# Kernel tuning notes

Measured on AMD Instinct MI355X. Metric: run time of the kernel, lower is better.

The kernel has to match this reference:

```python
import jax, jax.numpy as jnp
import numpy as np

MODEL_SIZE = 512
HEADS = 8
T = 2048
B = 2


def setup_inputs() -> dict:
    key = jax.random.key(0)
    ks = jax.random.split(key, 10)
    E = MODEL_SIZE
    w = 0.02  # weight init scale for numerical stability
    return {
        "input": jax.random.normal(ks[0], (T, B, E), jnp.float32),
        "pos": jax.random.normal(ks[1], (T, 1, E), jnp.float32),
        "in_proj_weight": jax.random.normal(ks[2], (3 * E, E), jnp.float32) * w,
        "out_proj_weight": jax.random.normal(ks[3], (E, E), jnp.float32) * w,
        "pos_proj_weight": jax.random.normal(ks[4], (E, E), jnp.float32) * w,
        "in_proj_bias": jax.random.normal(ks[5], (3 * E,), jnp.float32) * w,
        "out_proj_bias": jax.random.normal(ks[6], (E,), jnp.float32) * w,
        "pos_proj_bias": jax.random.normal(ks[7], (E,), jnp.float32) * w,
        "r_w_bias": jax.random.normal(ks[8], (HEADS, E // HEADS), jnp.float32) * w,
        "r_r_bias": jax.random.normal(ks[9], (HEADS, E // HEADS), jnp.float32) * w,
    }


def _rel_shift(x):
    # x: [B, H, T, R] -> Transformer-XL relative shift
    b, h, t, r = x.shape
    x = jnp.pad(x, ((0, 0), (0, 0), (0, 0), (1, 0)))  # [B,H,T,R+1]
    x = x.reshape(b, h, r + 1, t)[:, :, 1:, :]        # drop first row
    return x.reshape(b, h, t, r)


def reference(input, pos, in_proj_weight, out_proj_weight, pos_proj_weight,
              in_proj_bias, out_proj_bias, pos_proj_bias, r_w_bias, r_r_bias):
    t, b, e = input.shape
    h = r_w_bias.shape[0]
    d = e // h
    scale = 1.0 / np.sqrt(d).astype(np.float32)

    # fused QKV projection (time-first layout [T,B,E])
    qkv = input @ in_proj_weight.T + in_proj_bias          # [T,B,3E]
    q, k, v = jnp.split(qkv, 3, axis=-1)
    q = q.reshape(t, b, h, d)
    k = k.reshape(t, b, h, d)
    v = v.reshape(t, b, h, d)

    # relative position projection (pos batch dim is 1)
    r = (pos[:, 0] @ pos_proj_weight.T + pos_proj_bias).reshape(-1, h, d)  # [R,H,D]

    # content (AC) and position (BD) scores
    ac = jnp.einsum('tbhd,sbhd->bhts', q + r_w_bias, k)    # [B,H,T,T]
    bd = jnp.einsum('tbhd,rhd->bhtr', q + r_r_bias, r)     # [B,H,T,R]
    bd = _rel_shift(bd)[..., :t]

    attn = jax.nn.softmax((ac + bd) * scale, axis=-1)      # [B,H,T,T]
    ctx = jnp.einsum('bhts,sbhd->tbhd', attn, v).reshape(t, b, e)
    return ctx @ out_proj_weight.T + out_proj_bias
```

## Files before the change

### kernel.cpp

```cpp
#include <hip/hip_runtime.h>

#define T_SEQ 2048
#define BATCH 2
#define HEADS 8
#define DHEAD 64
#define EMB   512

typedef __attribute__((ext_vector_type(8))) short short8;
typedef __attribute__((ext_vector_type(4))) float floatx4;
typedef __attribute__((ext_vector_type(8))) unsigned short ushort8;
typedef __attribute__((ext_vector_type(4))) unsigned short ushort4v;

__device__ __forceinline__ unsigned short f2b(float f) {
    union { float f; unsigned u; } v; v.f = f;
    unsigned r = v.u + 0x7fffu + ((v.u >> 16) & 1u);
    return (unsigned short)(r >> 16);
}
__device__ __forceinline__ unsigned short f2bt(float f) {
    union { float f; unsigned u; } v; v.f = f;
    return (unsigned short)(v.u >> 16);
}
__device__ __forceinline__ float b2f(unsigned short s) {
    union { unsigned u; float f; } v; v.u = ((unsigned)s) << 16; return v.f;
}
__device__ __forceinline__ short8 ld_frag(const unsigned short* p) {
    ushort4v lo = *(const ushort4v*)p;
    ushort4v hi = *(const ushort4v*)(p + 4);
    short8 r;
    r[0] = lo[0]; r[1] = lo[1]; r[2] = lo[2]; r[3] = lo[3];
    r[4] = hi[0]; r[5] = hi[1]; r[6] = hi[2]; r[7] = hi[3];
    return r;
}
__device__ __forceinline__ void st8(unsigned short* p, ushort8 v) {
    ushort4v lo = { v[0], v[1], v[2], v[3] };
    ushort4v hi = { v[4], v[5], v[6], v[7] };
    *(ushort4v*)p = lo;
    *(ushort4v*)(p + 4) = hi;
}
#define MFMA16(a, b, c) __builtin_amdgcn_mfma_f32_16x16x32_bf16(a, b, c, 0, 0, 0)

__global__ __launch_bounds__(256)
void cvt_all(const float* __restrict__ s0, const float* __restrict__ s1,
             const float* __restrict__ s2, const float* __restrict__ s3,
             const float* __restrict__ s4,
             unsigned short* __restrict__ d0, unsigned short* __restrict__ d1,
             unsigned short* __restrict__ d2, unsigned short* __restrict__ d3,
             unsigned short* __restrict__ d4)
{
    const int i = blockIdx.x * 256 + threadIdx.x;
    const float* s; unsigned short* d; int off;
    if      (i <  524288) { s = s0; d = d0; off = i; }
    else if (i <  786432) { s = s1; d = d1; off = i -  524288; }
    else if (i <  983040) { s = s2; d = d2; off = i -  786432; }
    else if (i < 1048576) { s = s3; d = d3; off = i -  983040; }
    else if (i < 1114112) { s = s4; d = d4; off = i - 1048576; }
    else return;
    const float4 v = ((const float4*)s)[off];
    ushort4v o = { f2b(v.x), f2b(v.y), f2b(v.z), f2b(v.w) };
    ((ushort4v*)d)[off] = o;
}

__global__ __launch_bounds__(256)
void gemm_qkv_pos(const unsigned short* __restrict__ inb, const unsigned short* __restrict__ w_inb,
                  const float* __restrict__ b_in,
                  const unsigned short* __restrict__ posb, const unsigned short* __restrict__ w_posb,
                  const float* __restrict__ b_pos,
                  unsigned short* __restrict__ q_s, unsigned short* __restrict__ k_s,
                  unsigned short* __restrict__ vT, unsigned short* __restrict__ r_b)
{
    __shared__ unsigned short shmem[17408];
    unsigned short* As = shmem;
    unsigned short* Bs = shmem + 8704;
    unsigned short* tb = shmem;

    const int id = blockIdx.x;
    const bool isPos = (id >= 384);
    const int bx = isPos ? ((id - 384) & 3) : (id % 12);
    const int by = isPos ? ((id - 384) >> 2) : (id / 12);
    const unsigned short* A = isPos ? posb : inb;
    const unsigned short* B = isPos ? w_posb : w_inb;
    const float* bias = isPos ? b_pos : b_in;

    const int bm  = by * 128;
    const int bn  = bx * 128;
    const int tid = threadIdx.x;
    const int lane = tid & 63, w = tid >> 6;
    const int m16 = lane & 15, quad = lane >> 4;
    const int wm = (w & 1) * 64, wn = (w >> 1) * 64;

    floatx4 acc[4][4];
    #pragma unroll
    for (int i = 0; i < 4; ++i)
        #pragma unroll
        for (int j = 0; j < 4; ++j) acc[i][j] = (floatx4){0.f, 0.f, 0.f, 0.f};

    for (int k0 = 0; k0 < 512; k0 += 64) {
        #pragma unroll
        for (int s = tid; s < 1024; s += 256) {
            const int row = s >> 3, c = (s & 7) * 8;
            st8(&As[row * 68 + c], *(const ushort8*)(A + (size_t)(bm + row) * 512 + k0 + c));
            st8(&Bs[row * 68 + c], *(const ushort8*)(B + (size_t)(bn + row) * 512 + k0 + c));
        }
        __syncthreads();
        #pragma unroll
        for (int ks = 0; ks < 2; ++ks) {
            short8 af[4], bf[4];
            #pragma unroll
            for (int f = 0; f < 4; ++f) {
                af[f] = ld_frag(&As[(wm + f * 16 + m16) * 68 + ks * 32 + quad * 8]);
                bf[f] = ld_frag(&Bs[(wn + f * 16 + m16) * 68 + ks * 32 + quad * 8]);
            }
            #pragma unroll
            for (int fm = 0; fm < 4; ++fm)
                #pragma unroll
                for (int fn = 0; fn < 4; ++fn)
                    acc[fm][fn] = MFMA16(af[fm], bf[fn], acc[fm][fn]);
        }
        __syncthreads();
    }

    if (isPos) {
        #pragma unroll
        for (int fn = 0; fn < 4; ++fn) {
            const int n = bn + wn + fn * 16 + m16;
            const float bv = bias[n];
            #pragma unroll
            for (int fm = 0; fm < 4; ++fm)
                #pragma unroll
                for (int rgi = 0; rgi < 4; ++rgi) {
                    const int m = bm + wm + fm * 16 + quad * 4 + rgi;
                    r_b[(size_t)m * EMB + n] = f2b(acc[fm][fn][rgi] + bv);
                }
        }
    } else if (bn < 1024) {
        #pragma unroll
        for (int fn = 0; fn < 4; ++fn) {
            const int n = bn + wn + fn * 16 + m16;
            const float bv = bias[n];
            const int reg = n >> 9, c = n & 511, h = c >> 6, dd = c & 63;
            unsigned short* dst = reg == 0 ? q_s : k_s;
            #pragma unroll
            for (int fm = 0; fm < 4; ++fm)
                #pragma unroll
                for (int rgi = 0; rgi < 4; ++rgi) {
                    const int m = bm + wm + fm * 16 + quad * 4 + rgi;
                    const int t = m >> 1, b = m & 1;
                    dst[((size_t)(b * HEADS + h) * T_SEQ + t) * DHEAD + dd] = f2b(acc[fm][fn][rgi] + bv);
                }
        }
    } else {
        #pragma unroll
        for (int fn = 0; fn < 4; ++fn) {
            const int nl = wn + fn * 16 + m16;
            const float bv = bias[bn + nl];
            #pragma unroll
            for (int fm = 0; fm < 4; ++fm)
                #pragma unroll
                for (int rgi = 0; rgi < 4; ++rgi) {
                    const int ml = wm + fm * 16 + quad * 4 + rgi;
                    tb[nl * 131 + ml] = f2b(acc[fm][fn][rgi] + bv);
                }
        }
        __syncthreads();
        const int t0g = bm >> 1;
        for (int s2 = tid; s2 < 2048; s2 += 256) {
            const int nl = s2 >> 4;
            const int bsel = (s2 >> 3) & 1;
            const int j = s2 & 7;
            ushort8 o;
            #pragma unroll
            for (int k = 0; k < 8; ++k)
                o[k] = tb[nl * 131 + ((j * 8 + k) * 2 + bsel)];
            const int c = bn + nl - 1024, h = c >> 6, dd = c & 63;
            *(ushort8*)(vT + ((size_t)(bsel * HEADS + h) * DHEAD + dd) * T_SEQ + t0g + j * 8) = o;
        }
    }
}

__global__ __launch_bounds__(256)
void gemm_out(const unsigned short* __restrict__ A, const unsigned short* __restrict__ B,
              const float* __restrict__ bias, float* __restrict__ out)
{
    __shared__ unsigned short As[128 * 68];
    __shared__ unsigned short Bs[128 * 68];
    const int bm  = blockIdx.y * 128;
    const int bn  = blockIdx.x * 128;
    const int tid = threadIdx.x;
    const int lane = tid & 63, w = tid >> 6;
    const int m16 = lane & 15, quad = lane >> 4;
    const int wm = (w & 1) * 64, wn = (w >> 1) * 64;

    floatx4 acc[4][4];
    #pragma unroll
    for (int i = 0; i < 4; ++i)
        #pragma unroll
        for (int j = 0; j < 4; ++j) acc[i][j] = (floatx4){0.f, 0.f, 0.f, 0.f};

    for (int k0 = 0; k0 < 512; k0 += 64) {
        #pragma unroll
        for (int s = tid; s < 1024; s += 256) {
            const int row = s >> 3, c = (s & 7) * 8;
            st8(&As[row * 68 + c], *(const ushort8*)(A + (size_t)(bm + row) * 512 + k0 + c));
            st8(&Bs[row * 68 + c], *(const ushort8*)(B + (size_t)(bn + row) * 512 + k0 + c));
        }
        __syncthreads();
        #pragma unroll
        for (int ks = 0; ks < 2; ++ks) {
            short8 af[4], bf[4];
            #pragma unroll
            for (int f = 0; f < 4; ++f) {
                af[f] = ld_frag(&As[(wm + f * 16 + m16) * 68 + ks * 32 + quad * 8]);
                bf[f] = ld_frag(&Bs[(wn + f * 16 + m16) * 68 + ks * 32 + quad * 8]);
            }
            #pragma unroll
            for (int fm = 0; fm < 4; ++fm)
                #pragma unroll
                for (int fn = 0; fn < 4; ++fn)
                    acc[fm][fn] = MFMA16(af[fm], bf[fn], acc[fm][fn]);
        }
        __syncthreads();
    }

    #pragma unroll
    for (int fn = 0; fn < 4; ++fn) {
        const int n = bn + wn + fn * 16 + m16;
        const float bv = bias[n];
        #pragma unroll
        for (int fm = 0; fm < 4; ++fm)
            #pragma unroll
            for (int rgi = 0; rgi < 4; ++rgi) {
                const int m = bm + wm + fm * 16 + quad * 4 + rgi;
                out[(size_t)m * EMB + n] = acc[fm][fn][rgi] + bv;
            }
    }
}

__global__ __launch_bounds__(256)
void attn_mfma(const unsigned short* __restrict__ qg_, const unsigned short* __restrict__ kg_,
               const unsigned short* __restrict__ vtg_, const unsigned short* __restrict__ rg_,
               const float* __restrict__ rwb, const float* __restrict__ rrb,
               unsigned short* __restrict__ ctx)
{
    const int T   = T_SEQ;
    const int tb  = blockIdx.x;
    const int t0  = tb * 64;
    const int bh  = blockIdx.y;
    const int h   = bh & 7;
    const int b   = bh >> 3;
    const int tid = threadIdx.x;
    const int lane = tid & 63;
    const int w    = tid >> 6;
    const int m16  = lane & 15;
    const int quad = lane >> 4;
    const int ibase = 16 * w + quad * 4;

    __shared__ unsigned short lds[34624];
    unsigned short* ring  = lds + 26112;
    unsigned short* qrw_s = lds;
    unsigned short* qrr_s = lds + 8704;

    const unsigned short* qg  = qg_  + ((size_t)bh * T + t0) * DHEAD;
    const unsigned short* kg  = kg_  + (size_t)bh * T * DHEAD;
    const unsigned short* vtg = vtg_ + (size_t)bh * DHEAD * T;
    const unsigned short* rg  = rg_  + h * DHEAD;

    const float QSCALE = 0.125f * 1.44269504089f;
    for (int idx = tid; idx < 65 * 16; idx += 256) {
        const int row = idx >> 4, c = (idx & 15) << 2;
        ushort4v qv = {0, 0, 0, 0};
        if (t0 + row < T) qv = *(const ushort4v*)(qg + row * DHEAD + c);
        const float4 rr = *(const float4*)(rrb + h * DHEAD + c);
        qrr_s[row * 68 + c + 0] = f2b((b2f(qv[0]) + rr.x) * QSCALE);
        qrr_s[row * 68 + c + 1] = f2b((b2f(qv[1]) + rr.y) * QSCALE);
        qrr_s[row * 68 + c + 2] = f2b((b2f(qv[2]) + rr.z) * QSCALE);
        qrr_s[row * 68 + c + 3] = f2b((b2f(qv[3]) + rr.w) * QSCALE);
        if (row < 64) {
            const float4 rw = *(const float4*)(rwb + h * DHEAD + c);
            qrw_s[row * 68 + c + 0] = f2b((b2f(qv[0]) + rw.x) * QSCALE);
            qrw_s[row * 68 + c + 1] = f2b((b2f(qv[1]) + rw.y) * QSCALE);
            qrw_s[row * 68 + c + 2] = f2b((b2f(qv[2]) + rw.z) * QSCALE);
            qrw_s[row * 68 + c + 3] = f2b((b2f(qv[3]) + rw.w) * QSCALE);
        }
    }
    __syncthreads();

    short8 a_ac[2], a_qrl[2], a_qru[2];
    {
        const unsigned short* p0 = &qrw_s[(16 * w + m16) * 68 + quad * 8];
        a_ac[0]  = ld_frag(p0);  a_ac[1]  = ld_frag(p0 + 32);
        const unsigned short* p1 = &qrr_s[(16 * w + m16) * 68 + quad * 8];
        a_qrl[0] = ld_frag(p1);  a_qrl[1] = ld_frag(p1 + 32);
        const unsigned short* p2 = &qrr_s[(16 * w + 1 + m16) * 68 + quad * 8];
        a_qru[0] = ld_frag(p2);  a_qru[1] = ld_frag(p2 + 32);
    }

    const int srow0 = tid >> 3,          scol0 = (tid & 7) * 8;
    const int srow1 = (tid + 256) >> 3,  scol1 = (tid & 7) * 8;

    ushort8 kr[2], vr[2], rr8[2];
    auto prefetch = [&](int s0n) {
        const bool ln = (s0n <= t0);
        const int jb = (ln ? (s0n + T - t0 - 64) : (s0n - t0 - 65)) + 64;
        int j0 = jb + srow0; j0 = j0 < 0 ? 0 : (j0 > T - 1 ? T - 1 : j0);
        int j1 = jb + srow1; j1 = j1 < 0 ? 0 : (j1 > T - 1 ? T - 1 : j1);
        kr[0]  = *(const ushort8*)(kg + (size_t)(s0n + srow0) * DHEAD + scol0);
        kr[1]  = *(const ushort8*)(kg + (size_t)(s0n + srow1) * DHEAD + scol1);
        vr[0]  = *(const ushort8*)(vtg + (size_t)srow0 * T + s0n + scol0);
        vr[1]  = *(const ushort8*)(vtg + (size_t)srow1 * T + s0n + scol1);
        rr8[0] = *(const ushort8*)(rg + (size_t)j0 * EMB + scol0);
        rr8[1] = *(const ushort8*)(rg + (size_t)j1 * EMB + scol1);
    };
    auto store_bufs = [&](int q) {
        unsigned short* kb = lds + q * 4352;
        unsigned short* vb = lds + 8704 + q * 4352;
        unsigned short* rb = lds + 17408 + q * 4352;
        st8(&kb[srow0 * 68 + scol0], kr[0]);
        st8(&kb[srow1 * 68 + scol1], kr[1]);
        st8(&vb[srow0 * 68 + scol0], vr[0]);
        st8(&vb[srow1 * 68 + scol1], vr[1]);
        st8(&rb[srow0 * 68 + scol0], rr8[0]);
        st8(&rb[srow1 * 68 + scol1], rr8[1]);
    };
    auto stage_to = [&](unsigned short* dstb, int jbase) {
        #pragma unroll
        for (int idx = tid; idx < 512; idx += 256) {
            const int row = idx >> 3, c = (idx & 7) * 8;
            int j = jbase + row; j = j < 0 ? 0 : (j > T - 1 ? T - 1 : j);
            st8(&dstb[row * 68 + c], *(const ushort8*)(rg + (size_t)j * EMB + c));
        }
    };
    auto qr_half = [&](const unsigned short* rsb, const short8* aq, int slotbase) {
        #pragma unroll
        for (int cc = 0; cc < 4; ++cc) {
            floatx4 q4 = (floatx4){0.f, 0.f, 0.f, 0.f};
            #pragma unroll
            for (int ks = 0; ks < 2; ++ks) {
                short8 bfr = ld_frag(&rsb[(16 * cc + m16) * 68 + ks * 32 + quad * 8]);
                q4 = MFMA16(aq[ks], bfr, q4);
            }
            #pragma unroll
            for (int rgi = 0; rgi < 4; ++rgi)
                ring[(ibase + rgi) * 133 + slotbase + 16 * cc + m16] = f2bt(q4[rgi]);
        }
    };

    floatx4 O[4];
    float lrun[4];
    #pragma unroll
    for (int ct = 0; ct < 4; ++ct) O[ct] = (floatx4){0.f, 0.f, 0.f, 0.f};
    #pragma unroll
    for (int rgi = 0; rgi < 4; ++rgi) lrun[rgi] = 0.f;

    {
        stage_to(lds + 17408 + 4352, T - t0 - 64);
        prefetch(0);
        __syncthreads();
        qr_half(lds + 17408 + 4352, a_qrl, 0);
        store_bufs(0);
        __syncthreads();
    }

    for (int na = 0; na < T / 64; ++na) {
        const int s0 = na * 64;
        const int p = na & 1;
        unsigned short* kb = lds + p * 4352;
        unsigned short* vb = lds + 8704 + p * 4352;
        unsigned short* rp = lds + 17408 + p * 4352;
        const bool lower = (s0 <= t0);
        const int nph    = lower ? (s0 >> 6) : ((s0 - t0) >> 6);
        const int rbase  = (nph & 1) * 64;
        const int wbase  = 64 - rbase;
        const bool hasNext = (na + 1 < T / 64);

        floatx4 acf[4];
        #pragma unroll
        for (int ct = 0; ct < 4; ++ct) {
            acf[ct] = (floatx4){0.f, 0.f, 0.f, 0.f};
            #pragma unroll
            for (int ks = 0; ks < 2; ++ks) {
                short8 bfr = ld_frag(&kb[(16 * ct + m16) * 68 + ks * 32 + quad * 8]);
                acf[ct] = MFMA16(a_ac[ks], bfr, acf[ct]);
            }
        }
        qr_half(rp, lower ? a_qrl : a_qru, wbase);
        if (hasNext) prefetch(s0 + 64);
        __syncthreads();

        if (s0 != t0) {
            #pragma unroll
            for (int ct = 0; ct < 4; ++ct) {
                #pragma unroll
                for (int rgi = 0; rgi < 4; ++rgi) {
                    const int i = ibase + rgi;
                    const int slot = ((63 - i + 16 * ct + m16) + rbase) & 127;
                    acf[ct][rgi] += b2f(ring[i * 133 + slot]);
                }
            }
            if (s0 == t0 + 64 && lane == 48 && w == 3)
                acf[0][3] -= b2f(ring[63 * 133 + (rbase & 127)]);
        } else {
            #pragma unroll
            for (int ct = 0; ct < 4; ++ct) {
                #pragma unroll
                for (int rgi = 0; rgi < 4; ++rgi) {
                    const int i = ibase + rgi, u = 16 * ct + m16;
                    if (u <= i) acf[ct][rgi] += b2f(ring[i * 133 + (((63 - i + u) + rbase) & 127)]);
                }
            }
            unsigned short* rpo = lds + 17408 + (1 - p) * 4352;
            __syncthreads();
            stage_to(rpo, -1);
            __syncthreads();
            qr_half(rpo, a_qru, 64);
            __syncthreads();
            #pragma unroll
            for (int ct = 0; ct < 4; ++ct) {
                #pragma unroll
                for (int rgi = 0; rgi < 4; ++rgi) {
                    const int i = ibase + rgi, u = 16 * ct + m16;
                    if (u >= i + 2) acf[ct][rgi] += b2f(ring[i * 133 + 63 - i + u]);
                }
            }
        }

        #pragma unroll
        for (int rgi = 0; rgi < 4; ++rgi) {
            #pragma unroll
            for (int ct = 0; ct < 4; ++ct) {
                const float pv = exp2f(acf[ct][rgi]);
                acf[ct][rgi] = pv;
                lrun[rgi] += pv;
            }
        }
        #pragma unroll
        for (int ct = 0; ct < 4; ++ct)
            #pragma unroll
            for (int rgi = 0; rgi < 4; ++rgi)
                rp[(ibase + rgi) * 68 + 16 * ct + m16] = f2bt(acf[ct][rgi]);
        if (hasNext) store_bufs(1 - p);
        __syncthreads();

        short8 ap[2];
        {
            const unsigned short* pp = &rp[(16 * w + m16) * 68 + quad * 8];
            ap[0] = ld_frag(pp); ap[1] = ld_frag(pp + 32);
        }
        #pragma unroll
        for (int ct = 0; ct < 4; ++ct) {
            #pragma unroll
            for (int ks = 0; ks < 2; ++ks) {
                short8 bfr = ld_frag(&vb[(16 * ct + m16) * 68 + ks * 32 + quad * 8]);
                O[ct] = MFMA16(ap[ks], bfr, O[ct]);
            }
        }
    }

    #pragma unroll
    for (int rgi = 0; rgi < 4; ++rgi) {
        float l = lrun[rgi];
        #pragma unroll
        for (int off = 1; off < 16; off <<= 1)
            l += __shfl_xor(l, off);
        const float inv = 1.f / l;
        const int t = t0 + ibase + rgi;
        #pragma unroll
        for (int ct = 0; ct < 4; ++ct)
            ctx[((size_t)t * BATCH + b) * EMB + h * DHEAD + 16 * ct + m16] = f2bt(O[ct][rgi] * inv);
    }
}

extern "C" void kernel_launch(void* const* d_in, const int* in_sizes, int n_in,
                              void* d_out, int out_size, void* d_ws, size_t ws_size,
                              hipStream_t stream)
{
    const float* input = (const float*)d_in[0];
    const float* pos   = (const float*)d_in[1];
    const float* w_in  = (const float*)d_in[2];
    const float* w_out = (const float*)d_in[3];
    const float* w_pos = (const float*)d_in[4];
    const float* b_in  = (const float*)d_in[5];
    const float* b_out = (const float*)d_in[6];
    const float* b_pos = (const float*)d_in[7];
    const float* rwb   = (const float*)d_in[8];
    const float* rrb   = (const float*)d_in[9];

    unsigned short* ws     = (unsigned short*)d_ws;
    unsigned short* inb    = ws;
    unsigned short* posb   = ws + 2097152;
    unsigned short* w_inb  = ws + 3145728;
    unsigned short* w_posb = ws + 3932160;
    unsigned short* w_outb = ws + 6291456;
    unsigned short* q_s    = ws + 6553600;
    unsigned short* k_s    = ws + 8650752;
    unsigned short* vT     = ws + 10747904;
    unsigned short* r_b    = ws + 12845056;
    unsigned short* ctx_b  = ws + 13893632;

    cvt_all<<<4352, 256, 0, stream>>>(input, pos, w_in, w_pos, w_out,
                                      inb, posb, w_inb, w_posb, w_outb);
    gemm_qkv_pos<<<448, 256, 0, stream>>>(inb, w_inb, b_in, posb, w_posb, b_pos,
                                          q_s, k_s, vT, r_b);
    attn_mfma<<<dim3(32, 16), 256, 0, stream>>>(q_s, k_s, vT, r_b, rwb, rrb, ctx_b);
    gemm_out<<<dim3(4, 32), 256, 0, stream>>>(ctx_b, w_outb, b_out, (float*)d_out);
}
```

Baseline: 205.0 us.

## Split score MFMAs by key columns per wave, keeping all query rows in registers

Changes the work split of the QK^T and Q·R score MFMAs. Each wave now computes a 16-column slice of keys/positions for all 64 query rows, instead of 16 query rows against all 64 columns. The Q fragments (three sets of 4x2) are preloaded into registers and each wave loads only two K/R fragments from LDS per tile, cutting LDS fragment reads. The cost is a partial row-sum reduction across waves through LDS at the end, plus extra register pressure (24 short8 fragments and 16 running sums), which may lower occupancy.

```diff
diff --git a/kernel.cpp b/kernel.cpp
--- a/kernel.cpp
+++ b/kernel.cpp
@@ -252,7 +252,9 @@
     const int w    = tid >> 6;
     const int m16  = lane & 15;
     const int quad = lane >> 4;
-    const int ibase = 16 * w + quad * 4;
+    const int iq   = quad * 4;
+    const int u    = 16 * w + m16;
+    const int ibase = 16 * w + iq;
 
     __shared__ unsigned short lds[34624];
     unsigned short* ring  = lds + 26112;
@@ -284,14 +286,15 @@
     }
     __syncthreads();
 
-    short8 a_ac[2], a_qrl[2], a_qru[2];
-    {
-        const unsigned short* p0 = &qrw_s[(16 * w + m16) * 68 + quad * 8];
-        a_ac[0]  = ld_frag(p0);  a_ac[1]  = ld_frag(p0 + 32);
-        const unsigned short* p1 = &qrr_s[(16 * w + m16) * 68 + quad * 8];
-        a_qrl[0] = ld_frag(p1);  a_qrl[1] = ld_frag(p1 + 32);
-        const unsigned short* p2 = &qrr_s[(16 * w + 1 + m16) * 68 + quad * 8];
-        a_qru[0] = ld_frag(p2);  a_qru[1] = ld_frag(p2 + 32);
+    short8 a_ac[4][2], a_qrl[4][2], a_qru[4][2];
+    #pragma unroll
+    for (int rc = 0; rc < 4; ++rc) {
+        const unsigned short* p0 = &qrw_s[(rc * 16 + m16) * 68 + quad * 8];
+        a_ac[rc][0]  = ld_frag(p0);  a_ac[rc][1]  = ld_frag(p0 + 32);
+        const unsigned short* p1 = &qrr_s[(rc * 16 + m16) * 68 + quad * 8];
+        a_qrl[rc][0] = ld_frag(p1);  a_qrl[rc][1] = ld_frag(p1 + 32);
+        const unsigned short* p2 = &qrr_s[(rc * 16 + 1 + m16) * 68 + quad * 8];
+        a_qru[rc][0] = ld_frag(p2);  a_qru[rc][1] = ld_frag(p2 + 32);
     }
 
     const int srow0 = tid >> 3,          scol0 = (tid & 7) * 8;
@@ -329,27 +332,26 @@
             st8(&dstb[row * 68 + c], *(const ushort8*)(rg + (size_t)j * EMB + c));
         }
     };
-    auto qr_half = [&](const unsigned short* rsb, const short8* aq, int slotbase) {
-        #pragma unroll
-        for (int cc = 0; cc < 4; ++cc) {
+    auto qr_half = [&](const unsigned short* rsb, const short8 (*aq)[2], int slotbase) {
+        short8 rfr0 = ld_frag(&rsb[(16 * w + m16) * 68 + quad * 8]);
+        short8 rfr1 = ld_frag(&rsb[(16 * w + m16) * 68 + 32 + quad * 8]);
+        #pragma unroll
+        for (int rc = 0; rc < 4; ++rc) {
             floatx4 q4 = (floatx4){0.f, 0.f, 0.f, 0.f};
-            #pragma unroll
-            for (int ks = 0; ks < 2; ++ks) {
-                short8 bfr = ld_frag(&rsb[(16 * cc + m16) * 68 + ks * 32 + quad * 8]);
-                q4 = MFMA16(aq[ks], bfr, q4);
-            }
+            q4 = MFMA16(aq[rc][0], rfr0, q4);
+            q4 = MFMA16(aq[rc][1], rfr1, q4);
             #pragma unroll
             for (int rgi = 0; rgi < 4; ++rgi)
-                ring[(ibase + rgi) * 133 + slotbase + 16 * cc + m16] = f2bt(q4[rgi]);
+                ring[(rc * 16 + iq + rgi) * 133 + slotbase + u] = f2bt(q4[rgi]);
         }
     };
 
     floatx4 O[4];
-    float lrun[4];
+    float lrun[16];
     #pragma unroll
     for (int ct = 0; ct < 4; ++ct) O[ct] = (floatx4){0.f, 0.f, 0.f, 0.f};
     #pragma unroll
-    for (int rgi = 0; rgi < 4; ++rgi) lrun[rgi] = 0.f;
+    for (int i = 0; i < 16; ++i) lrun[i] = 0.f;
 
     {
         stage_to(lds + 17408 + 4352, T - t0 - 64);
@@ -373,13 +375,14 @@
         const bool hasNext = (na + 1 < T / 64);
 
         floatx4 acf[4];
-        #pragma unroll
-        for (int ct = 0; ct < 4; ++ct) {
-            acf[ct] = (floatx4){0.f, 0.f, 0.f, 0.f};
-            #pragma unroll
-            for (int ks = 0; ks < 2; ++ks) {
-                short8 bfr = ld_frag(&kb[(16 * ct + m16) * 68 + ks * 32 + quad * 8]);
-                acf[ct] = MFMA16(a_ac[ks], bfr, acf[ct]);
+        {
+            short8 kfr0 = ld_frag(&kb[(16 * w + m16) * 68 + quad * 8]);
+            short8 kfr1 = ld_frag(&kb[(16 * w + m16) * 68 + 32 + quad * 8]);
+            #pragma unroll
+            for (int rc = 0; rc < 4; ++rc) {
+                acf[rc] = (floatx4){0.f, 0.f, 0.f, 0.f};
+                acf[rc] = MFMA16(a_ac[rc][0], kfr0, acf[rc]);
+                acf[rc] = MFMA16(a_ac[rc][1], kfr1, acf[rc]);
             }
         }
         qr_half(rp, lower ? a_qrl : a_qru, wbase);
@@ -388,23 +391,23 @@
 
         if (s0 != t0) {
             #pragma unroll
-            for (int ct = 0; ct < 4; ++ct) {
+            for (int rc = 0; rc < 4; ++rc) {
                 #pragma unroll
                 for (int rgi = 0; rgi < 4; ++rgi) {
-                    const int i = ibase + rgi;
-                    const int slot = ((63 - i + 16 * ct + m16) + rbase) & 127;
-                    acf[ct][rgi] += b2f(ring[i * 133 + slot]);
+                    const int i = rc * 16 + iq + rgi;
+                    const int slot = ((63 - i + u) + rbase) & 127;
+                    acf[rc][rgi] += b2f(ring[i * 133 + slot]);
                 }
             }
-            if (s0 == t0 + 64 && lane == 48 && w == 3)
-                acf[0][3] -= b2f(ring[63 * 133 + (rbase & 127)]);
+            if (s0 == t0 + 64 && w == 0 && lane == 48)
+                acf[3][3] -= b2f(ring[63 * 133 + (rbase & 127)]);
         } else {
             #pragma unroll
-            for (int ct = 0; ct < 4; ++ct) {
+            for (int rc = 0; rc < 4; ++rc) {
                 #pragma unroll
                 for (int rgi = 0; rgi < 4; ++rgi) {
-                    const int i = ibase + rgi, u = 16 * ct + m16;
-                    if (u <= i) acf[ct][rgi] += b2f(ring[i * 133 + (((63 - i + u) + rbase) & 127)]);
+                    const int i = rc * 16 + iq + rgi;
+                    if (u <= i) acf[rc][rgi] += b2f(ring[i * 133 + (((63 - i + u) + rbase) & 127)]);
                 }
             }
             unsigned short* rpo = lds + 17408 + (1 - p) * 4352;
@@ -414,29 +417,29 @@
             qr_half(rpo, a_qru, 64);
             __syncthreads();
             #pragma unroll
-            for (int ct = 0; ct < 4; ++ct) {
+            for (int rc = 0; rc < 4; ++rc) {
                 #pragma unroll
                 for (int rgi = 0; rgi < 4; ++rgi) {
-                    const int i = ibase + rgi, u = 16 * ct + m16;
-                    if (u >= i + 2) acf[ct][rgi] += b2f(ring[i * 133 + 63 - i + u]);
+                    const int i = rc * 16 + iq + rgi;
+                    if (u >= i + 2) acf[rc][rgi] += b2f(ring[i * 133 + 63 - i + u]);
                 }
             }
         }
 
         #pragma unroll
-        for (int rgi = 0; rgi < 4; ++rgi) {
-            #pragma unroll
-            for (int ct = 0; ct < 4; ++ct) {
-                const float pv = exp2f(acf[ct][rgi]);
-                acf[ct][rgi] = pv;
-                lrun[rgi] += pv;
-            }
-        }
-        #pragma unroll
-        for (int ct = 0; ct < 4; ++ct)
+        for (int rc = 0; rc < 4; ++rc) {
+            #pragma unroll
+            for (int rgi = 0; rgi < 4; ++rgi) {
+                const float pv = exp2f(acf[rc][rgi]);
+                acf[rc][rgi] = pv;
+                lrun[rc * 4 + rgi] += pv;
+            }
+        }
+        #pragma unroll
+        for (int rc = 0; rc < 4; ++rc)
             #pragma unroll
             for (int rgi = 0; rgi < 4; ++rgi)
-                rp[(ibase + rgi) * 68 + 16 * ct + m16] = f2bt(acf[ct][rgi]);
+                rp[(rc * 16 + iq + rgi) * 68 + u] = f2bt(acf[rc][rgi]);
         if (hasNext) store_bufs(1 - p);
         __syncthreads();
 
@@ -455,14 +458,24 @@
         }
     }
 
+    float* lsum = (float*)ring;
+    #pragma unroll
+    for (int rc = 0; rc < 4; ++rc) {
+        #pragma unroll
+        for (int rgi = 0; rgi < 4; ++rgi) {
+            float v = lrun[rc * 4 + rgi];
+            v += __shfl_xor(v, 1); v += __shfl_xor(v, 2);
+            v += __shfl_xor(v, 4); v += __shfl_xor(v, 8);
+            if (m16 == 0) lsum[w * 64 + rc * 16 + iq + rgi] = v;
+        }
+    }
+    __syncthreads();
     #pragma unroll
     for (int rgi = 0; rgi < 4; ++rgi) {
-        float l = lrun[rgi];
-        #pragma unroll
-        for (int off = 1; off < 16; off <<= 1)
-            l += __shfl_xor(l, off);
+        const int i = ibase + rgi;
+        const float l = lsum[i] + lsum[64 + i] + lsum[128 + i] + lsum[192 + i];
         const float inv = 1.f / l;
-        const int t = t0 + ibase + rgi;
+        const int t = t0 + i;
         #pragma unroll
         for (int ct = 0; ct < 4; ++ct)
             ctx[((size_t)t * BATCH + b) * EMB + h * DHEAD + 16 * ct + m16] = f2bt(O[ct][rgi] * inv);
```

Result: slower. 262.0 us (+27.8%).

## Double-buffer LDS tiles with register prefetch in projection GEMMs

Applied to the files above, without the earlier changes.

Both the QKV/pos projection GEMM and the output GEMM now prefetch the next K tile from global memory into registers while MFMAs run on the current LDS buffer, then store it into a second LDS buffer. This hides global load latency behind compute and removes one barrier per K step. LDS use per block doubles to about 68 KB, which may reduce occupancy. The QKV fetch lambda also contains redundant loads that the compiler should eliminate, since they are overwritten immediately.

```diff
diff --git a/kernel.cpp b/kernel.cpp
--- a/kernel.cpp
+++ b/kernel.cpp
@@ -68,9 +68,7 @@
                   unsigned short* __restrict__ q_s, unsigned short* __restrict__ k_s,
                   unsigned short* __restrict__ vT, unsigned short* __restrict__ r_b)
 {
-    __shared__ unsigned short shmem[17408];
-    unsigned short* As = shmem;
-    unsigned short* Bs = shmem + 8704;
+    __shared__ unsigned short shmem[34816];
     unsigned short* tb = shmem;
 
     const int id = blockIdx.x;
@@ -87,6 +85,7 @@
     const int lane = tid & 63, w = tid >> 6;
     const int m16 = lane & 15, quad = lane >> 4;
     const int wm = (w & 1) * 64, wn = (w >> 1) * 64;
+    const int srow = tid >> 1, scol = (tid & 1) * 32;
 
     floatx4 acc[4][4];
     #pragma unroll
@@ -94,14 +93,44 @@
         #pragma unroll
         for (int j = 0; j < 4; ++j) acc[i][j] = (floatx4){0.f, 0.f, 0.f, 0.f};
 
-    for (int k0 = 0; k0 < 512; k0 += 64) {
-        #pragma unroll
-        for (int s = tid; s < 1024; s += 256) {
-            const int row = s >> 3, c = (s & 7) * 8;
-            st8(&As[row * 68 + c], *(const ushort8*)(A + (size_t)(bm + row) * 512 + k0 + c));
-            st8(&Bs[row * 68 + c], *(const ushort8*)(B + (size_t)(bn + row) * 512 + k0 + c));
-        }
-        __syncthreads();
+    ushort8 ar[4], br[4];
+    auto fetch = [&](int k0) {
+        #pragma unroll
+        for (int c = 0; c < 2; ++c) {
+            ar[c * 2 + 0] = *(const ushort8*)(A + (size_t)(bm + srow) * 512 + k0 + scol + c * 8);
+            ar[c * 2 + 1] = *(const ushort8*)(A + (size_t)(bm + 128 + srow - 128) * 512 + k0 + scol + c * 8);
+        }
+        ar[0] = *(const ushort8*)(A + (size_t)(bm + srow) * 512 + k0 + scol);
+        ar[1] = *(const ushort8*)(A + (size_t)(bm + srow) * 512 + k0 + scol + 8);
+        ar[2] = *(const ushort8*)(A + (size_t)(bm + srow) * 512 + k0 + scol + 16);
+        ar[3] = *(const ushort8*)(A + (size_t)(bm + srow) * 512 + k0 + scol + 24);
+        br[0] = *(const ushort8*)(B + (size_t)(bn + srow) * 512 + k0 + scol);
+        br[1] = *(const ushort8*)(B + (size_t)(bn + srow) * 512 + k0 + scol + 8);
+        br[2] = *(const ushort8*)(B + (size_t)(bn + srow) * 512 + k0 + scol + 16);
+        br[3] = *(const ushort8*)(B + (size_t)(bn + srow) * 512 + k0 + scol + 24);
+    };
+    auto store_stage = [&](int q) {
+        unsigned short* As = shmem + q * 17408;
+        unsigned short* Bs = shmem + q * 17408 + 8704;
+        st8(&As[srow * 68 + scol +  0], ar[0]);
+        st8(&As[srow * 68 + scol +  8], ar[1]);
+        st8(&As[srow * 68 + scol + 16], ar[2]);
+        st8(&As[srow * 68 + scol + 24], ar[3]);
+        st8(&Bs[srow * 68 + scol +  0], br[0]);
+        st8(&Bs[srow * 68 + scol +  8], br[1]);
+        st8(&Bs[srow * 68 + scol + 16], br[2]);
+        st8(&Bs[srow * 68 + scol + 24], br[3]);
+    };
+
+    fetch(0);
+    store_stage(0);
+    __syncthreads();
+
+    for (int kt = 0; kt < 8; ++kt) {
+        const int p = kt & 1;
+        unsigned short* As = shmem + p * 17408;
+        unsigned short* Bs = shmem + p * 17408 + 8704;
+        if (kt + 1 < 8) fetch((kt + 1) * 64);
         #pragma unroll
         for (int ks = 0; ks < 2; ++ks) {
             short8 af[4], bf[4];
@@ -116,6 +145,7 @@
                 for (int fn = 0; fn < 4; ++fn)
                     acc[fm][fn] = MFMA16(af[fm], bf[fn], acc[fm][fn]);
         }
+        if (kt + 1 < 8) store_stage(1 - p);
         __syncthreads();
     }
 
@@ -181,14 +211,14 @@
 void gemm_out(const unsigned short* __restrict__ A, const unsigned short* __restrict__ B,
               const float* __restrict__ bias, float* __restrict__ out)
 {
-    __shared__ unsigned short As[128 * 68];
-    __shared__ unsigned short Bs[128 * 68];
+    __shared__ unsigned short shmem[34816];
     const int bm  = blockIdx.y * 128;
     const int bn  = blockIdx.x * 128;
     const int tid = threadIdx.x;
     const int lane = tid & 63, w = tid >> 6;
     const int m16 = lane & 15, quad = lane >> 4;
     const int wm = (w & 1) * 64, wn = (w >> 1) * 64;
+    const int srow = tid >> 1, scol = (tid & 1) * 32;
 
     floatx4 acc[4][4];
     #pragma unroll
@@ -196,14 +226,39 @@
         #pragma unroll
         for (int j = 0; j < 4; ++j) acc[i][j] = (floatx4){0.f, 0.f, 0.f, 0.f};
 
-    for (int k0 = 0; k0 < 512; k0 += 64) {
-        #pragma unroll
-        for (int s = tid; s < 1024; s += 256) {
-            const int row = s >> 3, c = (s & 7) * 8;
-            st8(&As[row * 68 + c], *(const ushort8*)(A + (size_t)(bm + row) * 512 + k0 + c));
-            st8(&Bs[row * 68 + c], *(const ushort8*)(B + (size_t)(bn + row) * 512 + k0 + c));
-        }
-        __syncthreads();
+    ushort8 ar[4], br[4];
+    auto fetch = [&](int k0) {
+        ar[0] = *(const ushort8*)(A + (size_t)(bm + srow) * 512 + k0 + scol);
+        ar[1] = *(const ushort8*)(A + (size_t)(bm + srow) * 512 + k0 + scol + 8);
+        ar[2] = *(const ushort8*)(A + (size_t)(bm + srow) * 512 + k0 + scol + 16);
+        ar[3] = *(const ushort8*)(A + (size_t)(bm + srow) * 512 + k0 + scol + 24);
+        br[0] = *(const ushort8*)(B + (size_t)(bn + srow) * 512 + k0 + scol);
+        br[1] = *(const ushort8*)(B + (size_t)(bn + srow) * 512 + k0 + scol + 8);
+        br[2] = *(const ushort8*)(B + (size_t)(bn + srow) * 512 + k0 + scol + 16);
+        br[3] = *(const ushort8*)(B + (size_t)(bn + srow) * 512 + k0 + scol + 24);
+    };
+    auto store_stage = [&](int q) {
+        unsigned short* As = shmem + q * 17408;
+        unsigned short* Bs = shmem + q * 17408 + 8704;
+        st8(&As[srow * 68 + scol +  0], ar[0]);
+        st8(&As[srow * 68 + scol +  8], ar[1]);
+        st8(&As[srow * 68 + scol + 16], ar[2]);
+        st8(&As[srow * 68 + scol + 24], ar[3]);
+        st8(&Bs[srow * 68 + scol +  0], br[0]);
+        st8(&Bs[srow * 68 + scol +  8], br[1]);
+        st8(&Bs[srow * 68 + scol + 16], br[2]);
+        st8(&Bs[srow * 68 + scol + 24], br[3]);
+    };
+
+    fetch(0);
+    store_stage(0);
+    __syncthreads();
+
+    for (int kt = 0; kt < 8; ++kt) {
+        const int p = kt & 1;
+        unsigned short* As = shmem + p * 17408;
+        unsigned short* Bs = shmem + p * 17408 + 8704;
+        if (kt + 1 < 8) fetch((kt + 1) * 64);
         #pragma unroll
         for (int ks = 0; ks < 2; ++ks) {
             short8 af[4], bf[4];
@@ -218,6 +273,7 @@
                 for (int fn = 0; fn < 4; ++fn)
                     acc[fm][fn] = MFMA16(af[fm], bf[fn], acc[fm][fn]);
         }
+        if (kt + 1 < 8) store_stage(1 - p);
         __syncthreads();
     }
 
```

Measured after the change: 194.8 us. -5.0%, faster.
